# Kernel tuning notes

Hardware: AMD Instinct MI355X
Metric: run time of the kernel (lower is better)

## Reference

```python
import jax, jax.numpy as jnp
import numpy as np

B, N, D, Kp = 32, 4096, 128, 256  # batch*heads, seq_len, head_dim, linformer proj dim


def setup_inputs() -> dict:
    key = jax.random.key(0)
    ks = jax.random.split(key, 7)
    return {
        "Q": jax.random.normal(ks[0], (B, N, D), dtype=jnp.float32),
        "K": jax.random.normal(ks[1], (B, N, D), dtype=jnp.float32),
        "V": jax.random.normal(ks[2], (B, N, D), dtype=jnp.float32),
        "E_W": jax.random.normal(ks[3], (Kp, N), dtype=jnp.float32) * (1.0 / np.sqrt(N)),
        "E_b": jax.random.normal(ks[4], (Kp,), dtype=jnp.float32) * 0.02,
        "F_W": jax.random.normal(ks[5], (Kp, N), dtype=jnp.float32) * (1.0 / np.sqrt(N)),
        "F_b": jax.random.normal(ks[6], (Kp,), dtype=jnp.float32) * 0.02,
    }


def reference(Q, K, V, E_W, E_b, F_W, F_b):
    d = Q.shape[-1]
    scale = 1.0 / jnp.sqrt(jnp.asarray(d, Q.dtype))
    # E projection on K^T: [B,d,n] @ W^T -> [B,d,k]
    K_proj = jnp.einsum('bnd,kn->bdk', K, E_W) + E_b  # bias broadcasts over k axis
    # scaled scores [B,n,k], softmax over projected dim k
    scores = jnp.einsum('bnd,bdk->bnk', Q, K_proj) * scale
    P_bar = jax.nn.softmax(scores, axis=-1)
    # F projection on V^T then transpose back: [B,k,d]
    V_proj = jnp.einsum('bnd,kn->bkd', V, F_W) + F_b[:, None]
    # [B,n,k] @ [B,k,d] -> [B,n,d]
    return jnp.einsum('bnk,bkd->bnd', P_bar, V_proj)
```

## Files before the change

kernel.cpp:

```cpp
#include <hip/hip_runtime.h>
#include <cstdint>
#include <cstddef>

#define N_SEQ 4096
#define D_HEAD 128
#define KP_DIM 256

typedef __attribute__((ext_vector_type(4))) float f32x4;
typedef __attribute__((ext_vector_type(8))) short bf16x8;
typedef __attribute__((ext_vector_type(4))) short s16x4;
typedef __attribute__((ext_vector_type(2))) unsigned int u32x2;

static __device__ __forceinline__ short f2bf(float f) {
  uint32_t u = __builtin_bit_cast(uint32_t, f);
  u += 0x7FFFu + ((u >> 16) & 1u);
  return (short)(u >> 16);
}

static __device__ __forceinline__ unsigned int cvtpk(float a, float b) {
  unsigned int r;
  asm("v_cvt_pk_bf16_f32 %0, %1, %2" : "=v"(r) : "v"(a), "v"(b));
  return r;
}

static __device__ __forceinline__ int swz8(int r) { return (r ^ (r >> 2)) & 7; }

__global__ __launch_bounds__(256) void conv_w_kernel(
    const float* __restrict__ EW, const float* __restrict__ FW,
    short* __restrict__ wbf) {
  const int idx = blockIdx.x * 256 + threadIdx.x;
  const int half = 262144;
  f32x4 v = (idx < half) ? *(const f32x4*)(EW + (size_t)idx * 4)
                         : *(const f32x4*)(FW + (size_t)(idx - half) * 4);
  u32x2 h = {cvtpk(v[0], v[1]), cvtpk(v[2], v[3])};
  *(u32x2*)(wbf + (size_t)idx * 4) = h;
}

__global__ __launch_bounds__(512) void proj_partial_kernel(
    const float* __restrict__ Kin, const float* __restrict__ Vin,
    const short* __restrict__ wbf, float* __restrict__ pws) {
  const int bid = blockIdx.x;
  const int wk = (bid & 7) * 32 + (bid >> 3);
  const int b = wk & 31;
  const int s = (wk >> 5) & 3;
  const int p = wk >> 7;

  const float* __restrict__ X = (p == 0 ? Kin : Vin) + (size_t)b * (N_SEQ * D_HEAD);
  const short* __restrict__ wp = wbf + (size_t)p * (KP_DIM * N_SEQ);
  float* __restrict__ outp = pws + ((((size_t)b * 2 + p) * 4) + s) * (KP_DIM * D_HEAD);

  __shared__ __align__(16) short lw[2][KP_DIM * 64];
  __shared__ __align__(16) short xt[2][D_HEAD * 64];

  const int t = threadIdx.x;
  const int lane = t & 63;
  const int w = t >> 6;
  const int wm = (w >> 1) * 64;
  const int wn = (w & 1) * 64;
  const int l15 = lane & 15;
  const int l4 = lane >> 4;
  const int dq = t & 31;
  const int ng = t >> 5;

  const int n0 = s * 1024;

  f32x4 acc[4][4];
#pragma unroll
  for (int i = 0; i < 4; ++i)
#pragma unroll
    for (int j = 0; j < 4; ++j) acc[i][j] = (f32x4){0.f, 0.f, 0.f, 0.f};

  f32x4 xreg[4];

#pragma unroll
  for (int i = 0; i < 4; ++i)
    xreg[i] = *(const f32x4*)(X + (size_t)(n0 + ng * 4 + i) * D_HEAD + dq * 4);
#pragma unroll
  for (int i = 0; i < 4; ++i) {
    int g = t + i * 512;
    int row = g >> 3, c = g & 7;
    __builtin_amdgcn_global_load_lds(
        (const __attribute__((address_space(1))) void*)(wp + (size_t)row * N_SEQ + n0 +
                                                        ((c ^ swz8(row)) << 3)),
        (__attribute__((address_space(3))) void*)(&lw[0][g * 8]), 16, 0, 0);
  }
  asm volatile("s_waitcnt vmcnt(4)" ::: "memory");
#pragma unroll
  for (int j = 0; j < 4; ++j) {
    int drow = dq * 4 + j;
    u32x2 hv = {cvtpk(xreg[0][j], xreg[1][j]), cvtpk(xreg[2][j], xreg[3][j])};
    *(u32x2*)(&xt[0][drow * 64 + ((ng * 4) ^ (swz8(drow) << 3))]) = hv;
  }
  asm volatile("s_waitcnt vmcnt(0)" ::: "memory");
  __syncthreads();

  for (int it = 0; it < 16; ++it) {
    const int cur = it & 1, nxt = cur ^ 1;
    if (it < 15) {
      const int nc = n0 + (it + 1) * 64;
#pragma unroll
      for (int i = 0; i < 4; ++i)
        xreg[i] = *(const f32x4*)(X + (size_t)(nc + ng * 4 + i) * D_HEAD + dq * 4);
#pragma unroll
      for (int i = 0; i < 4; ++i) {
        int g = t + i * 512;
        int row = g >> 3, c = g & 7;
        __builtin_amdgcn_global_load_lds(
            (const __attribute__((address_space(1))) void*)(wp + (size_t)row * N_SEQ + nc +
                                                            ((c ^ swz8(row)) << 3)),
            (__attribute__((address_space(3))) void*)(&lw[nxt][g * 8]), 16, 0, 0);
      }
    }
#pragma unroll
    for (int ks2 = 0; ks2 < 2; ++ks2) {
      const int col0 = ks2 * 32 + l4 * 8;
      bf16x8 a[4], bb[4];
#pragma unroll
      for (int mt = 0; mt < 4; ++mt) {
        int row = wm + mt * 16 + l15;
        a[mt] = *(const bf16x8*)(&lw[cur][row * 64 + (col0 ^ (swz8(row) << 3))]);
      }
#pragma unroll
      for (int nt = 0; nt < 4; ++nt) {
        int row = wn + nt * 16 + l15;
        bb[nt] = *(const bf16x8*)(&xt[cur][row * 64 + (col0 ^ (swz8(row) << 3))]);
      }
#pragma unroll
      for (int mt = 0; mt < 4; ++mt)
#pragma unroll
        for (int nt = 0; nt < 4; ++nt)
          acc[mt][nt] = __builtin_amdgcn_mfma_f32_16x16x32_bf16(a[mt], bb[nt], acc[mt][nt], 0, 0, 0);
    }
    if (it < 15) {
      asm volatile("s_waitcnt vmcnt(4)" ::: "memory");
#pragma unroll
      for (int j = 0; j < 4; ++j) {
        int drow = dq * 4 + j;
        u32x2 hv = {cvtpk(xreg[0][j], xreg[1][j]), cvtpk(xreg[2][j], xreg[3][j])};
        *(u32x2*)(&xt[nxt][drow * 64 + ((ng * 4) ^ (swz8(drow) << 3))]) = hv;
      }
      asm volatile("s_waitcnt vmcnt(0)" ::: "memory");
    }
    __syncthreads();
  }

#pragma unroll
  for (int mt = 0; mt < 4; ++mt)
#pragma unroll
    for (int nt = 0; nt < 4; ++nt)
#pragma unroll
      for (int r = 0; r < 4; ++r) {
        int kk = wm + mt * 16 + l4 * 4 + r;
        int dd = wn + nt * 16 + l15;
        outp[kk * D_HEAD + dd] = acc[mt][nt][r];
      }
}

__global__ __launch_bounds__(256) void reduce_bias_kernel(
    const float* __restrict__ pws, const float* __restrict__ Eb,
    const float* __restrict__ Fb, short* __restrict__ kp, short* __restrict__ vpt) {
  const int sub = blockIdx.x & 3;
  const int b = blockIdx.x >> 2;
  const int t = threadIdx.x;
  __shared__ short tile[128 * 128];
  if (sub < 2) {
    const float* __restrict__ base = pws + ((size_t)b * 2) * 4 * 32768;
    const int off = sub * 16384;
    for (int i = t; i < 16384; i += 256) {
      int ii = off + i;
      int k = ii >> 7;
      float v = base[ii] + base[ii + 32768] + base[ii + 65536] + base[ii + 98304] + Eb[k];
      kp[(size_t)b * 32768 + ii] = f2bf(v);
    }
  } else {
    const int kh = sub - 2;
    const float* __restrict__ base = pws + (((size_t)b * 2 + 1) * 4) * 32768 + kh * 16384;
    for (int i = t; i < 16384; i += 256) {
      int kl = i >> 7, d = i & 127;
      float v = base[i] + base[i + 32768] + base[i + 65536] + base[i + 98304] + Fb[kh * 128 + kl];
      tile[kl * 128 + (d ^ ((kl & 15) << 3))] = f2bf(v);
    }
    __syncthreads();
    for (int i = t; i < 16384; i += 256) {
      int d = i >> 7, kl = i & 127;
      vpt[(size_t)b * 32768 + d * 256 + kh * 128 + kl] = tile[kl * 128 + (d ^ ((kl & 15) << 3))];
    }
  }
}

__global__ __launch_bounds__(512, 2) void attn_kernel(
    const float* __restrict__ Q, const short* __restrict__ kp,
    const short* __restrict__ vpt, float* __restrict__ out) {
  const int b = blockIdx.x >> 3;
  const int slice = blockIdx.x & 7;
  const int t = threadIdx.x;
  const int lane = t & 63;
  const int w = t >> 6;
  const int l15 = lane & 15, l4 = lane >> 4;

  __shared__ __align__(16) short lkp[256 * 128];
  __shared__ __align__(16) short lvpt[128 * 256];
  __shared__ __align__(16) short lp[8][1024];

  const short* __restrict__ kpb = kp + (size_t)b * 32768;
  const short* __restrict__ vptb = vpt + (size_t)b * 32768;

#pragma unroll
  for (int i = 0; i < 8; ++i) {
    int g = (w * 8 + i) * 64 + lane;
    int row = g >> 4, c = g & 15;
    __builtin_amdgcn_global_load_lds(
        (const __attribute__((address_space(1))) void*)(kpb + (size_t)row * 128 +
                                                        ((c ^ (row & 7)) << 3)),
        (__attribute__((address_space(3))) void*)(&lkp[g * 8]), 16, 0, 0);
  }
#pragma unroll
  for (int i = 0; i < 8; ++i) {
    int g = (w * 8 + i) * 64 + lane;
    int row = g >> 5, c = g & 31;
    __builtin_amdgcn_global_load_lds(
        (const __attribute__((address_space(1))) void*)(vptb + (size_t)row * 256 +
                                                        ((c ^ (row & 7)) << 3)),
        (__attribute__((address_space(3))) void*)(&lvpt[g * 8]), 16, 0, 0);
  }
  asm volatile("s_waitcnt vmcnt(0)" ::: "memory");
  __syncthreads();

  short* lpw = &lp[w][0];
  const float scale = 0.08838834764831845f;
  f32x4 qA[8], qB[8];

#define QLOAD(DST, TILE_I)                                                          \
  do {                                                                              \
    const float* qr_ = Q + ((size_t)b * N_SEQ + slice * 512 + (TILE_I) * 128 +      \
                            w * 16 + l15) * D_HEAD;                                 \
    _Pragma("unroll") for (int ks_ = 0; ks_ < 4; ++ks_) {                           \
      DST[2 * ks_] = *(const f32x4*)(qr_ + ks_ * 32 + l4 * 8);                      \
      DST[2 * ks_ + 1] = *(const f32x4*)(qr_ + ks_ * 32 + l4 * 8 + 4);              \
    }                                                                               \
  } while (0)

#define TILE_BODY(QC, QN, TILE_I, PREF)                                             \
  do {                                                                              \
    bf16x8 qf[4];                                                                   \
    _Pragma("unroll") for (int ks = 0; ks < 4; ++ks) {                              \
      union { unsigned int u[4]; bf16x8 v; } cv_;                                   \
      cv_.u[0] = cvtpk(QC[2 * ks][0], QC[2 * ks][1]);                               \
      cv_.u[1] = cvtpk(QC[2 * ks][2], QC[2 * ks][3]);                               \
      cv_.u[2] = cvtpk(QC[2 * ks + 1][0], QC[2 * ks + 1][1]);                       \
      cv_.u[3] = cvtpk(QC[2 * ks + 1][2], QC[2 * ks + 1][3]);                       \
      qf[ks] = cv_.v;                                                               \
    }                                                                               \
    if (PREF) QLOAD(QN, (TILE_I) + 1);                                              \
    f32x4 accs[16];                                                                 \
    _Pragma("unroll") for (int i = 0; i < 16; ++i)                                  \
        accs[i] = (f32x4){0.f, 0.f, 0.f, 0.f};                                      \
    _Pragma("unroll") for (int ks = 0; ks < 4; ++ks) {                              \
      _Pragma("unroll") for (int nt = 0; nt < 16; ++nt) {                           \
        bf16x8 af = *(const bf16x8*)(&lkp[(nt * 16 + l15) * 128 +                   \
                                          (((ks * 4 + l4) ^ (l15 & 7)) << 3)]);     \
        accs[nt] = __builtin_amdgcn_mfma_f32_16x16x32_bf16(af, qf[ks], accs[nt],    \
                                                           0, 0, 0);                \
      }                                                                             \
    }                                                                               \
    float m_ = -1e30f;                                                              \
    _Pragma("unroll") for (int nt = 0; nt < 16; ++nt)                               \
        _Pragma("unroll") for (int r = 0; r < 4; ++r) {                             \
      float v_ = accs[nt][r] * scale;                                               \
      accs[nt][r] = v_;                                                             \
      m_ = fmaxf(m_, v_);                                                           \
    }                                                                               \
    m_ = fmaxf(m_, __shfl_xor(m_, 16));                                             \
    m_ = fmaxf(m_, __shfl_xor(m_, 32));                                             \
    float s_ = 0.f;                                                                 \
    _Pragma("unroll") for (int nt = 0; nt < 16; ++nt)                               \
        _Pragma("unroll") for (int r = 0; r < 4; ++r) {                             \
      float e_ = __expf(accs[nt][r] - m_);                                          \
      accs[nt][r] = e_;                                                             \
      s_ += e_;                                                                     \
    }                                                                               \
    s_ += __shfl_xor(s_, 16);                                                       \
    s_ += __shfl_xor(s_, 32);                                                       \
    float inv_ = 1.0f / s_;                                                         \
    f32x4 acco[8];                                                                  \
    _Pragma("unroll") for (int i = 0; i < 8; ++i)                                   \
        acco[i] = (f32x4){0.f, 0.f, 0.f, 0.f};                                      \
    _Pragma("unroll") for (int qq = 0; qq < 4; ++qq) {                              \
      _Pragma("unroll") for (int ntl = 0; ntl < 4; ++ntl) {                         \
        int nt = qq * 4 + ntl;                                                      \
        unsigned int p0 = cvtpk(accs[nt][0] * inv_, accs[nt][1] * inv_);            \
        unsigned int p1 = cvtpk(accs[nt][2] * inv_, accs[nt][3] * inv_);            \
        int cw = 2 * ntl + (l4 >> 1);                                               \
        *(u32x2*)((char*)lpw + l15 * 128 + ((cw ^ (l15 & 7)) << 4) +                \
                  (l4 & 1) * 8) = (u32x2){p0, p1};                                  \
      }                                                                             \
      _Pragma("unroll") for (int ksl = 0; ksl < 2; ++ksl) {                         \
        bf16x8 pa = *(const bf16x8*)((char*)lpw + l15 * 128 +                       \
                                     (((4 * ksl + l4) ^ (l15 & 7)) << 4));          \
        int ksa = qq * 2 + ksl;                                                     \
        _Pragma("unroll") for (int ntv = 0; ntv < 8; ++ntv) {                       \
          bf16x8 bv = *(const bf16x8*)(&lvpt[(ntv * 16 + l15) * 256 +               \
                                             (((ksa * 4 + l4) ^ (l15 & 7)) << 3)]); \
          acco[ntv] = __builtin_amdgcn_mfma_f32_16x16x32_bf16(pa, bv, acco[ntv],    \
                                                              0, 0, 0);             \
        }                                                                           \
      }                                                                             \
    }                                                                               \
    float* ob_ = out + ((size_t)b * N_SEQ + slice * 512 + (TILE_I) * 128 +          \
                        w * 16) * D_HEAD;                                           \
    _Pragma("unroll") for (int ntv = 0; ntv < 8; ++ntv)                             \
        _Pragma("unroll") for (int r = 0; r < 4; ++r)                               \
            ob_[(size_t)(l4 * 4 + r) * D_HEAD + ntv * 16 + l15] = acco[ntv][r];     \
  } while (0)

  QLOAD(qA, 0);
  TILE_BODY(qA, qB, 0, 1);
  TILE_BODY(qB, qA, 1, 1);
  TILE_BODY(qA, qB, 2, 1);
  TILE_BODY(qB, qA, 3, 0);
#undef QLOAD
#undef TILE_BODY
}

extern "C" void kernel_launch(void* const* d_in, const int* in_sizes, int n_in,
                              void* d_out, int out_size, void* d_ws, size_t ws_size,
                              hipStream_t stream) {
  const float* Q  = (const float*)d_in[0];
  const float* K  = (const float*)d_in[1];
  const float* V  = (const float*)d_in[2];
  const float* EW = (const float*)d_in[3];
  const float* Eb = (const float*)d_in[4];
  const float* FW = (const float*)d_in[5];
  const float* Fb = (const float*)d_in[6];
  float* out = (float*)d_out;

  short* wbf = (short*)d_out;
  float* pws = (float*)d_out + 2097152;
  short* kpb = (short*)d_ws;
  short* vpt = (short*)((char*)d_ws + (size_t)32 * KP_DIM * D_HEAD * 2);

  conv_w_kernel<<<dim3(2048), dim3(256), 0, stream>>>(EW, FW, wbf);
  proj_partial_kernel<<<dim3(256), dim3(512), 0, stream>>>(K, V, wbf, pws);
  reduce_bias_kernel<<<dim3(128), dim3(256), 0, stream>>>(pws, Eb, Fb, kpb, vpt);
  attn_kernel<<<dim3(256), dim3(512), 0, stream>>>(Q, kpb, vpt, out);
}
```

Baseline: 103.5 us.

## Process two 16-row Q tiles per wave to reuse LDS fragments

Each wave now computes two 16-row query tiles at once (32 rows per wave, two rounds of 256 rows), so every K_proj and V_proj fragment read from LDS feeds two MFMAs instead of one. The softmax scale is folded into Q before the bf16 conversion, and block indices are remapped so that adjacent blocks work on different batches. The per-wave P staging buffer doubles in size. Register pressure roughly doubles for the accumulators, which under launch_bounds(512,2) risks spills, and the Q prefetch that previously overlapped loads with compute is gone.

Measured after the change: 116.2 us. +12.2%, slower.

```diff
diff --git a/kernel.cpp b/kernel.cpp
--- a/kernel.cpp
+++ b/kernel.cpp
@@ -191,8 +191,10 @@
 __global__ __launch_bounds__(512, 2) void attn_kernel(
     const float* __restrict__ Q, const short* __restrict__ kp,
     const short* __restrict__ vpt, float* __restrict__ out) {
-  const int b = blockIdx.x >> 3;
-  const int slice = blockIdx.x & 7;
+  const int bid = blockIdx.x;
+  const int wk = (bid & 7) * 32 + (bid >> 3);
+  const int b = wk >> 3;
+  const int slice = wk & 7;
   const int t = threadIdx.x;
   const int lane = t & 63;
   const int w = t >> 6;
@@ -200,7 +202,7 @@
 
   __shared__ __align__(16) short lkp[256 * 128];
   __shared__ __align__(16) short lvpt[128 * 256];
-  __shared__ __align__(16) short lp[8][1024];
+  __shared__ __align__(16) short lp[8][2048];
 
   const short* __restrict__ kpb = kp + (size_t)b * 32768;
   const short* __restrict__ vptb = vpt + (size_t)b * 32768;
@@ -228,98 +230,128 @@
 
   short* lpw = &lp[w][0];
   const float scale = 0.08838834764831845f;
-  f32x4 qA[8], qB[8];
-
-#define QLOAD(DST, TILE_I)                                                          \
-  do {                                                                              \
-    const float* qr_ = Q + ((size_t)b * N_SEQ + slice * 512 + (TILE_I) * 128 +      \
-                            w * 16 + l15) * D_HEAD;                                 \
-    _Pragma("unroll") for (int ks_ = 0; ks_ < 4; ++ks_) {                           \
-      DST[2 * ks_] = *(const f32x4*)(qr_ + ks_ * 32 + l4 * 8);                      \
-      DST[2 * ks_ + 1] = *(const f32x4*)(qr_ + ks_ * 32 + l4 * 8 + 4);              \
-    }                                                                               \
-  } while (0)
-
-#define TILE_BODY(QC, QN, TILE_I, PREF)                                             \
-  do {                                                                              \
-    bf16x8 qf[4];                                                                   \
-    _Pragma("unroll") for (int ks = 0; ks < 4; ++ks) {                              \
-      union { unsigned int u[4]; bf16x8 v; } cv_;                                   \
-      cv_.u[0] = cvtpk(QC[2 * ks][0], QC[2 * ks][1]);                               \
-      cv_.u[1] = cvtpk(QC[2 * ks][2], QC[2 * ks][3]);                               \
-      cv_.u[2] = cvtpk(QC[2 * ks + 1][0], QC[2 * ks + 1][1]);                       \
-      cv_.u[3] = cvtpk(QC[2 * ks + 1][2], QC[2 * ks + 1][3]);                       \
-      qf[ks] = cv_.v;                                                               \
-    }                                                                               \
-    if (PREF) QLOAD(QN, (TILE_I) + 1);                                              \
-    f32x4 accs[16];                                                                 \
-    _Pragma("unroll") for (int i = 0; i < 16; ++i)                                  \
-        accs[i] = (f32x4){0.f, 0.f, 0.f, 0.f};                                      \
-    _Pragma("unroll") for (int ks = 0; ks < 4; ++ks) {                              \
-      _Pragma("unroll") for (int nt = 0; nt < 16; ++nt) {                           \
-        bf16x8 af = *(const bf16x8*)(&lkp[(nt * 16 + l15) * 128 +                   \
-                                          (((ks * 4 + l4) ^ (l15 & 7)) << 3)]);     \
-        accs[nt] = __builtin_amdgcn_mfma_f32_16x16x32_bf16(af, qf[ks], accs[nt],    \
-                                                           0, 0, 0);                \
-      }                                                                             \
-    }                                                                               \
-    float m_ = -1e30f;                                                              \
-    _Pragma("unroll") for (int nt = 0; nt < 16; ++nt)                               \
-        _Pragma("unroll") for (int r = 0; r < 4; ++r) {                             \
-      float v_ = accs[nt][r] * scale;                                               \
-      accs[nt][r] = v_;                                                             \
-      m_ = fmaxf(m_, v_);                                                           \
-    }                                                                               \
-    m_ = fmaxf(m_, __shfl_xor(m_, 16));                                             \
-    m_ = fmaxf(m_, __shfl_xor(m_, 32));                                             \
-    float s_ = 0.f;                                                                 \
-    _Pragma("unroll") for (int nt = 0; nt < 16; ++nt)                               \
-        _Pragma("unroll") for (int r = 0; r < 4; ++r) {                             \
-      float e_ = __expf(accs[nt][r] - m_);                                          \
-      accs[nt][r] = e_;                                                             \
-      s_ += e_;                                                                     \
-    }                                                                               \
-    s_ += __shfl_xor(s_, 16);                                                       \
-    s_ += __shfl_xor(s_, 32);                                                       \
-    float inv_ = 1.0f / s_;                                                         \
-    f32x4 acco[8];                                                                  \
-    _Pragma("unroll") for (int i = 0; i < 8; ++i)                                   \
-        acco[i] = (f32x4){0.f, 0.f, 0.f, 0.f};                                      \
-    _Pragma("unroll") for (int qq = 0; qq < 4; ++qq) {                              \
-      _Pragma("unroll") for (int ntl = 0; ntl < 4; ++ntl) {                         \
-        int nt = qq * 4 + ntl;                                                      \
-        unsigned int p0 = cvtpk(accs[nt][0] * inv_, accs[nt][1] * inv_);            \
-        unsigned int p1 = cvtpk(accs[nt][2] * inv_, accs[nt][3] * inv_);            \
-        int cw = 2 * ntl + (l4 >> 1);                                               \
-        *(u32x2*)((char*)lpw + l15 * 128 + ((cw ^ (l15 & 7)) << 4) +                \
-                  (l4 & 1) * 8) = (u32x2){p0, p1};                                  \
-      }                                                                             \
-      _Pragma("unroll") for (int ksl = 0; ksl < 2; ++ksl) {                         \
-        bf16x8 pa = *(const bf16x8*)((char*)lpw + l15 * 128 +                       \
-                                     (((4 * ksl + l4) ^ (l15 & 7)) << 4));          \
-        int ksa = qq * 2 + ksl;                                                     \
-        _Pragma("unroll") for (int ntv = 0; ntv < 8; ++ntv) {                       \
-          bf16x8 bv = *(const bf16x8*)(&lvpt[(ntv * 16 + l15) * 256 +               \
-                                             (((ksa * 4 + l4) ^ (l15 & 7)) << 3)]); \
-          acco[ntv] = __builtin_amdgcn_mfma_f32_16x16x32_bf16(pa, bv, acco[ntv],    \
-                                                              0, 0, 0);             \
-        }                                                                           \
-      }                                                                             \
-    }                                                                               \
-    float* ob_ = out + ((size_t)b * N_SEQ + slice * 512 + (TILE_I) * 128 +          \
-                        w * 16) * D_HEAD;                                           \
-    _Pragma("unroll") for (int ntv = 0; ntv < 8; ++ntv)                             \
-        _Pragma("unroll") for (int r = 0; r < 4; ++r)                               \
-            ob_[(size_t)(l4 * 4 + r) * D_HEAD + ntv * 16 + l15] = acco[ntv][r];     \
-  } while (0)
-
-  QLOAD(qA, 0);
-  TILE_BODY(qA, qB, 0, 1);
-  TILE_BODY(qB, qA, 1, 1);
-  TILE_BODY(qA, qB, 2, 1);
-  TILE_BODY(qB, qA, 3, 0);
-#undef QLOAD
-#undef TILE_BODY
+
+  for (int rd = 0; rd < 2; ++rd) {
+    const int rowBase = slice * 512 + rd * 256 + w * 32;
+
+    f32x4 qta[8], qtb[8];
+    const float* qra = Q + ((size_t)b * N_SEQ + rowBase + l15) * D_HEAD;
+    const float* qrb = qra + 16 * D_HEAD;
+#pragma unroll
+    for (int ks = 0; ks < 4; ++ks) {
+      qta[2 * ks] = *(const f32x4*)(qra + ks * 32 + l4 * 8);
+      qta[2 * ks + 1] = *(const f32x4*)(qra + ks * 32 + l4 * 8 + 4);
+    }
+#pragma unroll
+    for (int ks = 0; ks < 4; ++ks) {
+      qtb[2 * ks] = *(const f32x4*)(qrb + ks * 32 + l4 * 8);
+      qtb[2 * ks + 1] = *(const f32x4*)(qrb + ks * 32 + l4 * 8 + 4);
+    }
+    bf16x8 qfA[4], qfB[4];
+#pragma unroll
+    for (int ks = 0; ks < 4; ++ks) {
+      union { unsigned int u[4]; bf16x8 v; } ca, cb;
+      ca.u[0] = cvtpk(qta[2 * ks][0] * scale, qta[2 * ks][1] * scale);
+      ca.u[1] = cvtpk(qta[2 * ks][2] * scale, qta[2 * ks][3] * scale);
+      ca.u[2] = cvtpk(qta[2 * ks + 1][0] * scale, qta[2 * ks + 1][1] * scale);
+      ca.u[3] = cvtpk(qta[2 * ks + 1][2] * scale, qta[2 * ks + 1][3] * scale);
+      qfA[ks] = ca.v;
+      cb.u[0] = cvtpk(qtb[2 * ks][0] * scale, qtb[2 * ks][1] * scale);
+      cb.u[1] = cvtpk(qtb[2 * ks][2] * scale, qtb[2 * ks][3] * scale);
+      cb.u[2] = cvtpk(qtb[2 * ks + 1][0] * scale, qtb[2 * ks + 1][1] * scale);
+      cb.u[3] = cvtpk(qtb[2 * ks + 1][2] * scale, qtb[2 * ks + 1][3] * scale);
+      qfB[ks] = cb.v;
+    }
+
+    f32x4 accsA[16], accsB[16];
+#pragma unroll
+    for (int i = 0; i < 16; ++i) {
+      accsA[i] = (f32x4){0.f, 0.f, 0.f, 0.f};
+      accsB[i] = (f32x4){0.f, 0.f, 0.f, 0.f};
+    }
+#pragma unroll
+    for (int ks = 0; ks < 4; ++ks) {
+#pragma unroll
+      for (int nt = 0; nt < 16; ++nt) {
+        bf16x8 af = *(const bf16x8*)(&lkp[(nt * 16 + l15) * 128 +
+                                          (((ks * 4 + l4) ^ (l15 & 7)) << 3)]);
+        accsA[nt] = __builtin_amdgcn_mfma_f32_16x16x32_bf16(af, qfA[ks], accsA[nt], 0, 0, 0);
+        accsB[nt] = __builtin_amdgcn_mfma_f32_16x16x32_bf16(af, qfB[ks], accsB[nt], 0, 0, 0);
+      }
+    }
+
+    float mA = -1e30f, mB = -1e30f;
+#pragma unroll
+    for (int nt = 0; nt < 16; ++nt)
+#pragma unroll
+      for (int r = 0; r < 4; ++r) {
+        mA = fmaxf(mA, accsA[nt][r]);
+        mB = fmaxf(mB, accsB[nt][r]);
+      }
+    mA = fmaxf(mA, __shfl_xor(mA, 16)); mA = fmaxf(mA, __shfl_xor(mA, 32));
+    mB = fmaxf(mB, __shfl_xor(mB, 16)); mB = fmaxf(mB, __shfl_xor(mB, 32));
+    float sA = 0.f, sB = 0.f;
+#pragma unroll
+    for (int nt = 0; nt < 16; ++nt)
+#pragma unroll
+      for (int r = 0; r < 4; ++r) {
+        float eA = __expf(accsA[nt][r] - mA);
+        float eB = __expf(accsB[nt][r] - mB);
+        accsA[nt][r] = eA; accsB[nt][r] = eB;
+        sA += eA; sB += eB;
+      }
+    sA += __shfl_xor(sA, 16); sA += __shfl_xor(sA, 32);
+    sB += __shfl_xor(sB, 16); sB += __shfl_xor(sB, 32);
+    float invA = 1.0f / sA, invB = 1.0f / sB;
+
+    f32x4 accoA[8], accoB[8];
+#pragma unroll
+    for (int i = 0; i < 8; ++i) {
+      accoA[i] = (f32x4){0.f, 0.f, 0.f, 0.f};
+      accoB[i] = (f32x4){0.f, 0.f, 0.f, 0.f};
+    }
+#pragma unroll
+    for (int qq = 0; qq < 4; ++qq) {
+#pragma unroll
+      for (int ntl = 0; ntl < 4; ++ntl) {
+        int nt = qq * 4 + ntl;
+        int cw = 2 * ntl + (l4 >> 1);
+        unsigned int a0 = cvtpk(accsA[nt][0] * invA, accsA[nt][1] * invA);
+        unsigned int a1 = cvtpk(accsA[nt][2] * invA, accsA[nt][3] * invA);
+        *(u32x2*)((char*)lpw + l15 * 128 + ((cw ^ (l15 & 7)) << 4) + (l4 & 1) * 8) =
+            (u32x2){a0, a1};
+        unsigned int b0 = cvtpk(accsB[nt][0] * invB, accsB[nt][1] * invB);
+        unsigned int b1 = cvtpk(accsB[nt][2] * invB, accsB[nt][3] * invB);
+        *(u32x2*)((char*)lpw + (16 + l15) * 128 + ((cw ^ (l15 & 7)) << 4) + (l4 & 1) * 8) =
+            (u32x2){b0, b1};
+      }
+#pragma unroll
+      for (int ksl = 0; ksl < 2; ++ksl) {
+        bf16x8 paA = *(const bf16x8*)((char*)lpw + l15 * 128 +
+                                      (((4 * ksl + l4) ^ (l15 & 7)) << 4));
+        bf16x8 paB = *(const bf16x8*)((char*)lpw + (16 + l15) * 128 +
+                                      (((4 * ksl + l4) ^ (l15 & 7)) << 4));
+        int ksa = qq * 2 + ksl;
+#pragma unroll
+        for (int ntv = 0; ntv < 8; ++ntv) {
+          bf16x8 bv = *(const bf16x8*)(&lvpt[(ntv * 16 + l15) * 256 +
+                                             (((ksa * 4 + l4) ^ (l15 & 7)) << 3)]);
+          accoA[ntv] = __builtin_amdgcn_mfma_f32_16x16x32_bf16(paA, bv, accoA[ntv], 0, 0, 0);
+          accoB[ntv] = __builtin_amdgcn_mfma_f32_16x16x32_bf16(paB, bv, accoB[ntv], 0, 0, 0);
+        }
+      }
+    }
+
+    float* obA = out + ((size_t)b * N_SEQ + rowBase) * D_HEAD;
+    float* obB = obA + 16 * D_HEAD;
+#pragma unroll
+    for (int ntv = 0; ntv < 8; ++ntv)
+#pragma unroll
+      for (int r = 0; r < 4; ++r) {
+        obA[(size_t)(l4 * 4 + r) * D_HEAD + ntv * 16 + l15] = accoA[ntv][r];
+        obB[(size_t)(l4 * 4 + r) * D_HEAD + ntv * 16 + l15] = accoB[ntv][r];
+      }
+  }
 }
 
 extern "C" void kernel_launch(void* const* d_in, const int* in_sizes, int n_in,
```
